# Kernel tuning notes

Measured on AMD Instinct MI355X. Metric: run time of the kernel, lower is better.

The kernel has to match this reference:

```python
import jax, jax.numpy as jnp
import numpy as np

BITS = 4
GROUP_SIZE = 128
INF, OUTF, TOKENS = 4096, 11008, 256


def setup_inputs() -> dict:
    key = jax.random.key(0)
    k1, k2, k3, k4, k5 = jax.random.split(key, 5)
    n_groups = INF // GROUP_SIZE  # 32
    x = jax.random.normal(k1, (TOKENS, INF), dtype=jnp.float32)
    qweight = jax.random.randint(k2, (INF // 32 * BITS, OUTF), 0, 2**31 - 1, dtype=jnp.int32)
    qzeros = jax.random.randint(k3, (n_groups, OUTF // 32 * BITS), 0, 2**31 - 1, dtype=jnp.int32)
    scales = jax.random.uniform(k4, (n_groups, OUTF), dtype=jnp.float32, minval=1e-3, maxval=2e-2)
    bias = jax.random.normal(k5, (OUTF,), dtype=jnp.float32)
    return {"x": x, "qweight": qweight, "qzeros": qzeros, "scales": scales, "bias": bias}


def _dequantize(qweight, qzeros, scales):
    """Unpack int4 nibbles and build the fp32 weight [infeatures, outfeatures]."""
    shifts = jnp.arange(0, 32, BITS, dtype=jnp.int32)  # [8]
    mask = (1 << BITS) - 1
    out_f = qweight.shape[1]
    # qweight row packs 8 consecutive in-features -> [K, O] int in [0, 15]
    w = ((qweight[:, None, :] >> shifts[None, :, None]) & mask).reshape(-1, out_f)
    # qzeros col packs 8 consecutive out-features; stored as (zero - 1)
    n_groups = qzeros.shape[0]
    z = (((qzeros[:, :, None] >> shifts[None, None, :]) & mask) + 1).reshape(n_groups, out_f)
    g_idx = jnp.arange(w.shape[0], dtype=jnp.int32) // GROUP_SIZE  # [K]
    return (w - z[g_idx]).astype(jnp.float32) * scales[g_idx]


def reference(x, qweight, qzeros, scales, bias):
    W = _dequantize(qweight, qzeros, scales)  # [infeatures, outfeatures]
    return x @ W + bias  # [tokens, outfeatures]
```

## Files before the change

kernel.cpp:

```cpp
#include <hip/hip_runtime.h>
#include <stdint.h>

#define TOKENS  256
#define INF     4096
#define OUTF    11008
#define NGROUPS 32
#define KSPLIT  2
#define PHK     128
#define NPH     ((INF / KSPLIT) / PHK)
#define NTH     256

typedef __attribute__((ext_vector_type(2))) _Float16 f16x2;
typedef __attribute__((ext_vector_type(8))) _Float16 f16x8;
typedef __attribute__((ext_vector_type(2))) __fp16   pkh2;
typedef __attribute__((ext_vector_type(4))) float    f32x4;

union U32H2 { uint32_t u; f16x2 h; };
union H8    { f16x2 h2[4]; f16x8 h8; };
union PK    { pkh2 p; f16x2 h; };

__device__ __forceinline__ void gl2lds16(const void* g, void* l) {
    __builtin_amdgcn_global_load_lds(
        (const __attribute__((address_space(1))) uint32_t*)g,
        (__attribute__((address_space(3))) uint32_t*)l, 16, 0, 0);
}

__global__ __launch_bounds__(NTH)
void prep(const float* __restrict__ x, _Float16* __restrict__ x16,
          const float* __restrict__ bias, float* __restrict__ out) {
    const int b = blockIdx.x;
    if (b < 512) {
        const int t   = b * NTH + threadIdx.x;
        const int row = t >> 9;
        const int c   = t & 511;
        const float* p = x + (size_t)row * INF + c * 8;
        f32x4 v0 = *(const f32x4*)p;
        f32x4 v1 = *(const f32x4*)(p + 4);
        H8 o; PK k0, k1, k2, k3;
        k0.p = __builtin_amdgcn_cvt_pkrtz(v0[0], v1[0]);
        k1.p = __builtin_amdgcn_cvt_pkrtz(v0[1], v1[1]);
        k2.p = __builtin_amdgcn_cvt_pkrtz(v0[2], v1[2]);
        k3.p = __builtin_amdgcn_cvt_pkrtz(v0[3], v1[3]);
        o.h2[0] = k0.h; o.h2[1] = k1.h; o.h2[2] = k2.h; o.h2[3] = k3.h;
        *(f16x8*)(x16 + (size_t)row * INF + c * 8) = o.h8;
    } else {
        const int t = (b - 512) * NTH + threadIdx.x;
        const int c = t % (OUTF / 4);
        const int r = t / (OUTF / 4);
        const f32x4 bv = ((const f32x4*)bias)[c];
        ((f32x4*)out)[(size_t)r * (OUTF / 4) + c] = bv;
    }
}

__global__ __launch_bounds__(NTH, 2)
void qlin_main(const _Float16* __restrict__ x16,
               const uint32_t* __restrict__ qweight,
               const uint32_t* __restrict__ qzeros,
               const float* __restrict__ scales,
               float* __restrict__ out)
{
    __shared__ alignas(16) _Float16 As[2][128 * PHK];

    const int tid = threadIdx.x;

    const int d   = blockIdx.x;
    const int lin = (d & 7) * 43 + (d >> 3);
    const int bx   = lin >> 2;
    const int memb = lin & 3;
    const int by = memb >> 1;
    const int ks = memb & 1;

    const int lane = tid & 63;
    const int quad = lane >> 4;
    const int l16  = lane & 15;
    const int wv   = tid >> 6;

    const int rowoff = tid >> 4;
    const int chk    = tid & 15;
    const int row0   = by * 128;
    const uint32_t aoff = (uint32_t)((row0 + rowoff) * (INF * 2)
                                     + ks * (INF / KSPLIT) * 2
                                     + ((chk ^ rowoff) & 15) * 16);
    const char* x16b = (const char*)x16;
    _Float16* ldsW = &As[0][0];
    const int ldsSlotBase = wv * 512;

    const int col0 = bx * 128 + wv * 32 + l16;
    const int col1 = col0 + 16;
    const int bOff0 = quad * OUTF + col0;
    const int bOff1 = quad * OUTF + col1;
    const int zsh   = (col0 & 7) * 4;
    const int qrow0 = ks * (INF / KSPLIT / 8);
    const int g0    = ks * (NGROUPS / KSPLIT);

    f32x4 acc[8][2];
#pragma unroll
    for (int mi = 0; mi < 8; ++mi)
#pragma unroll
        for (int nf = 0; nf < 2; ++nf)
            acc[mi][nf] = f32x4{0.f, 0.f, 0.f, 0.f};

    uint32_t Breg[2][8];
    float    sS[2][2];
    uint32_t qZ[2][2];

#pragma unroll
    for (int r = 0; r < 8; ++r)
        gl2lds16(x16b + aoff + r * 131072, ldsW + r * 2048 + ldsSlotBase);
    __builtin_amdgcn_sched_barrier(0);
    {
        sS[0][0] = scales[g0 * OUTF + col0];
        sS[0][1] = scales[g0 * OUTF + col1];
        qZ[0][0] = qzeros[g0 * (OUTF / 8) + (col0 >> 3)];
        qZ[0][1] = qzeros[g0 * (OUTF / 8) + (col1 >> 3)];
        const uint32_t* qp = qweight + (size_t)qrow0 * OUTF;
#pragma unroll
        for (int s = 0; s < 4; ++s) {
            Breg[0][2 * s + 0] = qp[(size_t)(s * 4) * OUTF + bOff0];
            Breg[0][2 * s + 1] = qp[(size_t)(s * 4) * OUTF + bOff1];
        }
    }

#define PHASE_BODY(PAR, P, DO_PREFETCH)                                          \
    {                                                                            \
        __builtin_amdgcn_sched_barrier(0);                                       \
        asm volatile("s_waitcnt vmcnt(12)" ::: "memory");                        \
        __builtin_amdgcn_s_barrier();                                            \
        __builtin_amdgcn_sched_barrier(0);                                       \
        if (DO_PREFETCH) {                                                       \
            const int pn = (P) + 1;                                              \
            const uint32_t pb = (uint32_t)(pn * (PHK * 2));                      \
            _Float16* ldsN = ldsW + (1 - (PAR)) * 16384;                         \
            _Pragma("unroll")                                                    \
            for (int r = 0; r < 8; ++r)                                          \
                gl2lds16(x16b + aoff + r * 131072 + pb,                          \
                         ldsN + r * 2048 + ldsSlotBase);                         \
            __builtin_amdgcn_sched_barrier(0);           \
            const int gn = g0 + pn;                                              \
            sS[1 - (PAR)][0] = scales[gn * OUTF + col0];                         \
            sS[1 - (PAR)][1] = scales[gn * OUTF + col1];                         \
            qZ[1 - (PAR)][0] = qzeros[gn * (OUTF / 8) + (col0 >> 3)];            \
            qZ[1 - (PAR)][1] = qzeros[gn * (OUTF / 8) + (col1 >> 3)];            \
            const uint32_t* qpb = qweight + (size_t)(qrow0 + pn * 16) * OUTF;    \
            _Pragma("unroll")                                                    \
            for (int s = 0; s < 4; ++s) {                                        \
                Breg[1 - (PAR)][2 * s + 0] = qpb[(size_t)(s * 4) * OUTF + bOff0];\
                Breg[1 - (PAR)][2 * s + 1] = qpb[(size_t)(s * 4) * OUTF + bOff1];\
            }                                                                    \
        }                                                                        \
        f16x2 hs2[2], hz2[2];                                                    \
        _Pragma("unroll")                                                        \
        for (int nf = 0; nf < 2; ++nf) {                                         \
            const float s = sS[PAR][nf];                                         \
            const int   z = (int)((qZ[PAR][nf] >> zsh) & 15u) + 1025;            \
            const _Float16 hs = (_Float16)s;                                     \
            const _Float16 hz = (_Float16)(-(float)z);                           \
            hs2[nf] = f16x2{hs, hs};                                             \
            hz2[nf] = f16x2{hz, hz};                                             \
        }                                                                        \
        const _Float16* buf = ldsW + (PAR) * 16384;                              \
        _Pragma("unroll")                                                        \
        for (int s = 0; s < 4; ++s) {                                            \
            f16x8 af[8];                                                         \
            _Pragma("unroll")                                                    \
            for (int mi = 0; mi < 8; ++mi) {                                     \
                const int m  = mi * 16 + l16;                                    \
                const int sc = ((s * 4 + quad) ^ l16) & 15;                      \
                af[mi] = *(const f16x8*)(buf + m * PHK + sc * 8);                \
            }                                                                    \
            _Pragma("unroll")                                                    \
            for (int nf = 0; nf < 2; ++nf) {                                     \
                const uint32_t q = Breg[PAR][2 * s + nf];                        \
                H8 b;                                                            \
                _Pragma("unroll")                                                \
                for (int j = 0; j < 4; ++j) {                                    \
                    U32H2 u;                                                     \
                    u.u = ((q >> (4 * j)) & 0x000F000Fu) | 0x64006400u;          \
                    b.h2[j] = (u.h + hz2[nf]) * hs2[nf];                         \
                }                                                                \
                __builtin_amdgcn_s_setprio(1);                                   \
                _Pragma("unroll")                                                \
                for (int mi = 0; mi < 8; ++mi)                                   \
                    acc[mi][nf] = __builtin_amdgcn_mfma_f32_16x16x32_f16(        \
                        af[mi], b.h8, acc[mi][nf], 0, 0, 0);                     \
                __builtin_amdgcn_s_setprio(0);                                   \
            }                                                                    \
        }                                                                        \
    }

#pragma unroll 1
    for (int pp = 0; pp < NPH / 2; ++pp) {
        PHASE_BODY(0, 2 * pp, true)
        PHASE_BODY(1, 2 * pp + 1, (pp < NPH / 2 - 1))
    }
#undef PHASE_BODY

#pragma unroll
    for (int nf = 0; nf < 2; ++nf) {
        const int col = (nf == 0) ? col0 : col1;
#pragma unroll
        for (int mi = 0; mi < 8; ++mi) {
            const int r0 = by * 128 + mi * 16 + quad * 4;
#pragma unroll
            for (int rg = 0; rg < 4; ++rg)
                unsafeAtomicAdd(&out[(size_t)(r0 + rg) * OUTF + col],
                                acc[mi][nf][rg]);
        }
    }
}

__global__ __launch_bounds__(NTH, 2)
void qlin_fb(const float* __restrict__ x,
             const uint32_t* __restrict__ qweight,
             const uint32_t* __restrict__ qzeros,
             const float* __restrict__ scales,
             const float* __restrict__ bias,
             float* __restrict__ out)
{
    __shared__ alignas(16) _Float16 Asb[64][40];
    __shared__ alignas(16) _Float16 Bsb[128][40];
    const int tid = threadIdx.x;
    const int bx = blockIdx.x, by = blockIdx.y;
    const int am = tid >> 2, ar = tid & 3;
    const float* xrow = x + (size_t)(by * 64 + am) * INF + ar * 8;
    const int bc = tid & 127, br = tid >> 7;
    const int bn = bx * 128 + bc;
    const int bswz = (bc >> 3) & 3;
    const int lane = tid & 63, quad = lane >> 4, l16 = lane & 15;
    const int wv = tid >> 6, wm = wv >> 1, wn = wv & 1;
    f32x4 acc[2][4];
#pragma unroll
    for (int i = 0; i < 2; ++i)
#pragma unroll
        for (int j = 0; j < 4; ++j) acc[i][j] = f32x4{0.f, 0.f, 0.f, 0.f};
    f32x4 pa0 = *(const f32x4*)(xrow + 0);
    f32x4 pa1 = *(const f32x4*)(xrow + 4);
    uint32_t pq0 = qweight[(size_t)br * OUTF + bn];
    uint32_t pq1 = qweight[(size_t)(br + 2) * OUTF + bn];
    for (int g = 0; g < NGROUPS; ++g) {
        const float s = scales[g * OUTF + bn];
        const uint32_t qzv = qzeros[g * (OUTF / 8) + (bn >> 3)];
        const int z = (int)((qzv >> (4 * (bn & 7))) & 15u) + 1;
        const _Float16 hs = (_Float16)s;
        const _Float16 hz = (_Float16)(-(float)(1024 + z));
        const f16x2 hs2 = {hs, hs}, hz2 = {hz, hz};
#pragma unroll
        for (int t4 = 0; t4 < 4; ++t4) {
            const int it = (g << 2) + t4;
            { H8 ah; PK p0, p1, p2, p3;
              p0.p = __builtin_amdgcn_cvt_pkrtz(pa0[0], pa1[0]);
              p1.p = __builtin_amdgcn_cvt_pkrtz(pa0[1], pa1[1]);
              p2.p = __builtin_amdgcn_cvt_pkrtz(pa0[2], pa1[2]);
              p3.p = __builtin_amdgcn_cvt_pkrtz(pa0[3], pa1[3]);
              ah.h2[0] = p0.h; ah.h2[1] = p1.h; ah.h2[2] = p2.h; ah.h2[3] = p3.h;
              *(f16x8*)&Asb[am][ar * 8] = ah.h8; }
            { const uint32_t qq[2] = {pq0, pq1};
#pragma unroll
              for (int rr = 0; rr < 2; ++rr) {
                  const int r = br + rr * 2; H8 bh;
#pragma unroll
                  for (int jp = 0; jp < 4; ++jp) {
                      U32H2 u; u.u = ((qq[rr] >> (4 * jp)) & 0x000F000Fu) | 0x64006400u;
                      bh.h2[jp] = (u.h + hz2) * hs2;
                  }
                  *(f16x8*)&Bsb[bc][(r ^ bswz) * 8] = bh.h8;
              } }
            __syncthreads();
            const int itn = (it < 127) ? it + 1 : 127;
            pa0 = *(const f32x4*)(xrow + itn * 32);
            pa1 = *(const f32x4*)(xrow + itn * 32 + 4);
            pq0 = qweight[(size_t)(itn * 4 + br) * OUTF + bn];
            pq1 = qweight[(size_t)(itn * 4 + br + 2) * OUTF + bn];
            f16x8 af[2], bf[4];
#pragma unroll
            for (int mi = 0; mi < 2; ++mi)
                af[mi] = *(const f16x8*)&Asb[wm * 32 + mi * 16 + l16][quad * 8];
#pragma unroll
            for (int ni = 0; ni < 4; ++ni) {
                const int c = wn * 64 + ni * 16 + l16;
                bf[ni] = *(const f16x8*)&Bsb[c][(quad ^ ((c >> 3) & 3)) * 8];
            }
#pragma unroll
            for (int mi = 0; mi < 2; ++mi)
#pragma unroll
                for (int ni = 0; ni < 4; ++ni)
                    acc[mi][ni] = __builtin_amdgcn_mfma_f32_16x16x32_f16(
                        af[mi], bf[ni], acc[mi][ni], 0, 0, 0);
            __syncthreads();
        }
    }
#pragma unroll
    for (int ni = 0; ni < 4; ++ni) {
        const int col = bx * 128 + wn * 64 + ni * 16 + l16;
        const float bv = bias[col];
#pragma unroll
        for (int mi = 0; mi < 2; ++mi) {
            const int row0 = by * 64 + wm * 32 + mi * 16 + quad * 4;
#pragma unroll
            for (int rg = 0; rg < 4; ++rg)
                out[(size_t)(row0 + rg) * OUTF + col] = acc[mi][ni][rg] + bv;
        }
    }
}

extern "C" void kernel_launch(void* const* d_in, const int* in_sizes, int n_in,
                              void* d_out, int out_size, void* d_ws, size_t ws_size,
                              hipStream_t stream) {
    const float*    xx = (const float*)d_in[0];
    const uint32_t* qw = (const uint32_t*)d_in[1];
    const uint32_t* qz = (const uint32_t*)d_in[2];
    const float*    sc = (const float*)d_in[3];
    const float*    bs = (const float*)d_in[4];
    float* out = (float*)d_out;

    const size_t x16_bytes = (size_t)TOKENS * INF * sizeof(_Float16);
    if (ws_size >= x16_bytes) {
        _Float16* x16 = (_Float16*)d_ws;
        prep<<<512 + (TOKENS * OUTF / 4) / NTH, NTH, 0, stream>>>(xx, x16, bs, out);
        qlin_main<<<(OUTF / 128) * (TOKENS / 128) * KSPLIT, NTH, 0, stream>>>(
            x16, qw, qz, sc, out);
    } else {
        dim3 grid(OUTF / 128, TOKENS / 64);
        qlin_fb<<<grid, NTH, 0, stream>>>(xx, qw, qz, sc, bs, out);
    }
}
```

Baseline: 123.1 us.

## Drop split-K; tile 64 columns per block with per-wave private A tiles

Removes the K-split and its atomic-add epilogue. Each block now covers 128 rows by 64 columns over the full K, and each wave owns 32 rows by 64 columns with its own LDS slice, so the block-wide barrier goes away. The bias is added in the epilogue, so the prep kernel no longer initialises the output. In exchange, each wave loads twice as many packed weights per phase, there is less A reuse per B dequant, and the launch uses the same block count with longer per-block work.

```diff
diff --git a/kernel.cpp b/kernel.cpp
--- a/kernel.cpp
+++ b/kernel.cpp
@@ -5,9 +5,8 @@
 #define INF     4096
 #define OUTF    11008
 #define NGROUPS 32
-#define KSPLIT  2
 #define PHK     128
-#define NPH     ((INF / KSPLIT) / PHK)
+#define NPH     32
 #define NTH     256
 
 typedef __attribute__((ext_vector_type(2))) _Float16 f16x2;
@@ -26,30 +25,20 @@
 }
 
 __global__ __launch_bounds__(NTH)
-void prep(const float* __restrict__ x, _Float16* __restrict__ x16,
-          const float* __restrict__ bias, float* __restrict__ out) {
-    const int b = blockIdx.x;
-    if (b < 512) {
-        const int t   = b * NTH + threadIdx.x;
-        const int row = t >> 9;
-        const int c   = t & 511;
-        const float* p = x + (size_t)row * INF + c * 8;
-        f32x4 v0 = *(const f32x4*)p;
-        f32x4 v1 = *(const f32x4*)(p + 4);
-        H8 o; PK k0, k1, k2, k3;
-        k0.p = __builtin_amdgcn_cvt_pkrtz(v0[0], v1[0]);
-        k1.p = __builtin_amdgcn_cvt_pkrtz(v0[1], v1[1]);
-        k2.p = __builtin_amdgcn_cvt_pkrtz(v0[2], v1[2]);
-        k3.p = __builtin_amdgcn_cvt_pkrtz(v0[3], v1[3]);
-        o.h2[0] = k0.h; o.h2[1] = k1.h; o.h2[2] = k2.h; o.h2[3] = k3.h;
-        *(f16x8*)(x16 + (size_t)row * INF + c * 8) = o.h8;
-    } else {
-        const int t = (b - 512) * NTH + threadIdx.x;
-        const int c = t % (OUTF / 4);
-        const int r = t / (OUTF / 4);
-        const f32x4 bv = ((const f32x4*)bias)[c];
-        ((f32x4*)out)[(size_t)r * (OUTF / 4) + c] = bv;
-    }
+void prep(const float* __restrict__ x, _Float16* __restrict__ x16) {
+    const int t   = blockIdx.x * NTH + threadIdx.x;
+    const int row = t >> 9;
+    const int c   = t & 511;
+    const float* p = x + (size_t)row * INF + c * 8;
+    f32x4 v0 = *(const f32x4*)p;
+    f32x4 v1 = *(const f32x4*)(p + 4);
+    H8 o; PK k0, k1, k2, k3;
+    k0.p = __builtin_amdgcn_cvt_pkrtz(v0[0], v1[0]);
+    k1.p = __builtin_amdgcn_cvt_pkrtz(v0[1], v1[1]);
+    k2.p = __builtin_amdgcn_cvt_pkrtz(v0[2], v1[2]);
+    k3.p = __builtin_amdgcn_cvt_pkrtz(v0[3], v1[3]);
+    o.h2[0] = k0.h; o.h2[1] = k1.h; o.h2[2] = k2.h; o.h2[3] = k3.h;
+    *(f16x8*)(x16 + (size_t)row * INF + c * 8) = o.h8;
 }
 
 __global__ __launch_bounds__(NTH, 2)
@@ -57,100 +46,95 @@
                const uint32_t* __restrict__ qweight,
                const uint32_t* __restrict__ qzeros,
                const float* __restrict__ scales,
+               const float* __restrict__ bias,
                float* __restrict__ out)
 {
-    __shared__ alignas(16) _Float16 As[2][128 * PHK];
+    __shared__ alignas(16) _Float16 As[4][2][4096];
 
     const int tid = threadIdx.x;
 
     const int d   = blockIdx.x;
     const int lin = (d & 7) * 43 + (d >> 3);
-    const int bx   = lin >> 2;
-    const int memb = lin & 3;
-    const int by = memb >> 1;
-    const int ks = memb & 1;
+    const int bx  = lin >> 1;
+    const int by  = lin & 1;
 
     const int lane = tid & 63;
     const int quad = lane >> 4;
     const int l16  = lane & 15;
     const int wv   = tid >> 6;
 
-    const int rowoff = tid >> 4;
-    const int chk    = tid & 15;
-    const int row0   = by * 128;
-    const uint32_t aoff = (uint32_t)((row0 + rowoff) * (INF * 2)
-                                     + ks * (INF / KSPLIT) * 2
-                                     + ((chk ^ rowoff) & 15) * 16);
     const char* x16b = (const char*)x16;
-    _Float16* ldsW = &As[0][0];
-    const int ldsSlotBase = wv * 512;
-
-    const int col0 = bx * 128 + wv * 32 + l16;
-    const int col1 = col0 + 16;
-    const int bOff0 = quad * OUTF + col0;
-    const int bOff1 = quad * OUTF + col1;
-    const int zsh   = (col0 & 7) * 4;
-    const int qrow0 = ks * (INF / KSPLIT / 8);
-    const int g0    = ks * (NGROUPS / KSPLIT);
-
-    f32x4 acc[8][2];
-#pragma unroll
-    for (int mi = 0; mi < 8; ++mi)
-#pragma unroll
-        for (int nf = 0; nf < 2; ++nf)
+    const char* aBase = x16b + (size_t)(by * 128 + wv * 32 + quad) * (INF * 2);
+    uint32_t co[4];
+#pragma unroll
+    for (int rm = 0; rm < 4; ++rm)
+        co[rm] = (uint32_t)(((l16 ^ ((quad + rm * 4) & 15)) & 15) * 16);
+
+    int colN[4], bOffN[4], zOffN[4];
+#pragma unroll
+    for (int nf = 0; nf < 4; ++nf) {
+        colN[nf]  = bx * 64 + nf * 16 + l16;
+        bOffN[nf] = quad * OUTF + colN[nf];
+        zOffN[nf] = colN[nf] >> 3;
+    }
+    const int zsh = (l16 & 7) * 4;
+
+    f32x4 acc[2][4];
+#pragma unroll
+    for (int mi = 0; mi < 2; ++mi)
+#pragma unroll
+        for (int nf = 0; nf < 4; ++nf)
             acc[mi][nf] = f32x4{0.f, 0.f, 0.f, 0.f};
 
-    uint32_t Breg[2][8];
-    float    sS[2][2];
-    uint32_t qZ[2][2];
-
-#pragma unroll
-    for (int r = 0; r < 8; ++r)
-        gl2lds16(x16b + aoff + r * 131072, ldsW + r * 2048 + ldsSlotBase);
+    uint32_t Breg[2][16];
+    float    sS[2][4];
+    uint32_t qZ[2][4];
+
+#define LOAD_A(PN, BUF)                                                          \
+    {                                                                            \
+        const uint32_t pb_ = (uint32_t)((PN) * (PHK * 2));                       \
+        _Pragma("unroll")                                                        \
+        for (int r = 0; r < 8; ++r)                                              \
+            gl2lds16(aBase + r * 32768 + pb_ + co[r & 3],                        \
+                     &As[wv][BUF][r * 512]);                                     \
+    }
+
+#define LOAD_B(SLOT, PN)                                                         \
+    {                                                                            \
+        const int gn_ = (PN);                                                    \
+        _Pragma("unroll")                                                        \
+        for (int nf = 0; nf < 4; ++nf) {                                         \
+            sS[SLOT][nf] = scales[gn_ * OUTF + colN[nf]];                        \
+            qZ[SLOT][nf] = qzeros[gn_ * (OUTF / 8) + zOffN[nf]];                 \
+        }                                                                        \
+        const uint32_t* qpb_ = qweight + (size_t)((PN) * 16) * OUTF;             \
+        _Pragma("unroll")                                                        \
+        for (int s_ = 0; s_ < 4; ++s_)                                           \
+            _Pragma("unroll")                                                    \
+            for (int nf = 0; nf < 4; ++nf)                                       \
+                Breg[SLOT][s_ * 4 + nf] =                                        \
+                    qpb_[(size_t)(s_ * 4) * OUTF + bOffN[nf]];                   \
+    }
+
+    LOAD_A(0, 0)
     __builtin_amdgcn_sched_barrier(0);
-    {
-        sS[0][0] = scales[g0 * OUTF + col0];
-        sS[0][1] = scales[g0 * OUTF + col1];
-        qZ[0][0] = qzeros[g0 * (OUTF / 8) + (col0 >> 3)];
-        qZ[0][1] = qzeros[g0 * (OUTF / 8) + (col1 >> 3)];
-        const uint32_t* qp = qweight + (size_t)qrow0 * OUTF;
-#pragma unroll
-        for (int s = 0; s < 4; ++s) {
-            Breg[0][2 * s + 0] = qp[(size_t)(s * 4) * OUTF + bOff0];
-            Breg[0][2 * s + 1] = qp[(size_t)(s * 4) * OUTF + bOff1];
-        }
-    }
-
-#define PHASE_BODY(PAR, P, DO_PREFETCH)                                          \
+    LOAD_B(0, 0)
+
+#define PHASE_BODY(PAR, P, DO_PRE, WAIT0)                                        \
     {                                                                            \
+        const int p_ = (P);                                                      \
         __builtin_amdgcn_sched_barrier(0);                                       \
-        asm volatile("s_waitcnt vmcnt(12)" ::: "memory");                        \
-        __builtin_amdgcn_s_barrier();                                            \
+        if (WAIT0) { asm volatile("s_waitcnt vmcnt(0)" ::: "memory"); }          \
+        else       { asm volatile("s_waitcnt vmcnt(24)" ::: "memory"); }         \
         __builtin_amdgcn_sched_barrier(0);                                       \
-        if (DO_PREFETCH) {                                                       \
-            const int pn = (P) + 1;                                              \
-            const uint32_t pb = (uint32_t)(pn * (PHK * 2));                      \
-            _Float16* ldsN = ldsW + (1 - (PAR)) * 16384;                         \
-            _Pragma("unroll")                                                    \
-            for (int r = 0; r < 8; ++r)                                          \
-                gl2lds16(x16b + aoff + r * 131072 + pb,                          \
-                         ldsN + r * 2048 + ldsSlotBase);                         \
+        if (DO_PRE) {                                                            \
+            LOAD_A(p_ + 1, 1 - (PAR))                                            \
             __builtin_amdgcn_sched_barrier(0);           \
-            const int gn = g0 + pn;                                              \
-            sS[1 - (PAR)][0] = scales[gn * OUTF + col0];                         \
-            sS[1 - (PAR)][1] = scales[gn * OUTF + col1];                         \
-            qZ[1 - (PAR)][0] = qzeros[gn * (OUTF / 8) + (col0 >> 3)];            \
-            qZ[1 - (PAR)][1] = qzeros[gn * (OUTF / 8) + (col1 >> 3)];            \
-            const uint32_t* qpb = qweight + (size_t)(qrow0 + pn * 16) * OUTF;    \
-            _Pragma("unroll")                                                    \
-            for (int s = 0; s < 4; ++s) {                                        \
-                Breg[1 - (PAR)][2 * s + 0] = qpb[(size_t)(s * 4) * OUTF + bOff0];\
-                Breg[1 - (PAR)][2 * s + 1] = qpb[(size_t)(s * 4) * OUTF + bOff1];\
-            }                                                                    \
+            LOAD_B(1 - (PAR), p_ + 1)                                            \
         }                                                                        \
-        f16x2 hs2[2], hz2[2];                                                    \
-        _Pragma("unroll")                                                        \
-        for (int nf = 0; nf < 2; ++nf) {                                         \
+        f16x2 hs2[4], hz2[4];                                                    \
+        _Pragma("unroll")                                                        \
+        for (int nf = 0; nf < 4; ++nf) {                                         \
             const float s = sS[PAR][nf];                                         \
             const int   z = (int)((qZ[PAR][nf] >> zsh) & 15u) + 1025;            \
             const _Float16 hs = (_Float16)s;                                     \
@@ -158,19 +142,19 @@
             hs2[nf] = f16x2{hs, hs};                                             \
             hz2[nf] = f16x2{hz, hz};                                             \
         }                                                                        \
-        const _Float16* buf = ldsW + (PAR) * 16384;                              \
+        const _Float16* buf = &As[wv][PAR][0];                                   \
         _Pragma("unroll")                                                        \
         for (int s = 0; s < 4; ++s) {                                            \
-            f16x8 af[8];                                                         \
+            f16x8 af[2];                                                         \
             _Pragma("unroll")                                                    \
-            for (int mi = 0; mi < 8; ++mi) {                                     \
-                const int m  = mi * 16 + l16;                                    \
+            for (int mi = 0; mi < 2; ++mi) {                                     \
+                const int w  = mi * 16 + l16;                                    \
                 const int sc = ((s * 4 + quad) ^ l16) & 15;                      \
-                af[mi] = *(const f16x8*)(buf + m * PHK + sc * 8);                \
+                af[mi] = *(const f16x8*)(buf + w * PHK + sc * 8);                \
             }                                                                    \
             _Pragma("unroll")                                                    \
-            for (int nf = 0; nf < 2; ++nf) {                                     \
-                const uint32_t q = Breg[PAR][2 * s + nf];                        \
+            for (int nf = 0; nf < 4; ++nf) {                                     \
+                const uint32_t q = Breg[PAR][s * 4 + nf];                        \
                 H8 b;                                                            \
                 _Pragma("unroll")                                                \
                 for (int j = 0; j < 4; ++j) {                                    \
@@ -180,7 +164,7 @@
                 }                                                                \
                 __builtin_amdgcn_s_setprio(1);                                   \
                 _Pragma("unroll")                                                \
-                for (int mi = 0; mi < 8; ++mi)                                   \
+                for (int mi = 0; mi < 2; ++mi)                                   \
                     acc[mi][nf] = __builtin_amdgcn_mfma_f32_16x16x32_f16(        \
                         af[mi], b.h8, acc[mi][nf], 0, 0, 0);                     \
                 __builtin_amdgcn_s_setprio(0);                                   \
@@ -189,22 +173,26 @@
     }
 
 #pragma unroll 1
-    for (int pp = 0; pp < NPH / 2; ++pp) {
-        PHASE_BODY(0, 2 * pp, true)
-        PHASE_BODY(1, 2 * pp + 1, (pp < NPH / 2 - 1))
-    }
+    for (int pp = 0; pp < NPH / 2 - 1; ++pp) {
+        PHASE_BODY(0, 2 * pp, true, false)
+        PHASE_BODY(1, 2 * pp + 1, true, false)
+    }
+    PHASE_BODY(0, NPH - 2, true,  false)
+    PHASE_BODY(1, NPH - 1, false, true)
 #undef PHASE_BODY
-
-#pragma unroll
-    for (int nf = 0; nf < 2; ++nf) {
-        const int col = (nf == 0) ? col0 : col1;
-#pragma unroll
-        for (int mi = 0; mi < 8; ++mi) {
-            const int r0 = by * 128 + mi * 16 + quad * 4;
+#undef LOAD_A
+#undef LOAD_B
+
+#pragma unroll
+    for (int nf = 0; nf < 4; ++nf) {
+        const int col = colN[nf];
+        const float bv = bias[col];
+#pragma unroll
+        for (int mi = 0; mi < 2; ++mi) {
+            const int r0 = by * 128 + wv * 32 + mi * 16 + quad * 4;
 #pragma unroll
             for (int rg = 0; rg < 4; ++rg)
-                unsafeAtomicAdd(&out[(size_t)(r0 + rg) * OUTF + col],
-                                acc[mi][nf][rg]);
+                out[(size_t)(r0 + rg) * OUTF + col] = acc[mi][nf][rg] + bv;
         }
     }
 }
@@ -316,9 +304,9 @@
     const size_t x16_bytes = (size_t)TOKENS * INF * sizeof(_Float16);
     if (ws_size >= x16_bytes) {
         _Float16* x16 = (_Float16*)d_ws;
-        prep<<<512 + (TOKENS * OUTF / 4) / NTH, NTH, 0, stream>>>(xx, x16, bs, out);
-        qlin_main<<<(OUTF / 128) * (TOKENS / 128) * KSPLIT, NTH, 0, stream>>>(
-            x16, qw, qz, sc, out);
+        prep<<<(TOKENS * INF / 8) / NTH, NTH, 0, stream>>>(xx, x16);
+        qlin_main<<<(OUTF / 64) * (TOKENS / 128), NTH, 0, stream>>>(
+            x16, qw, qz, sc, bs, out);
     } else {
         dim3 grid(OUTF / 128, TOKENS / 64);
         qlin_fb<<<grid, NTH, 0, stream>>>(xx, qw, qz, sc, bs, out);
```

Result: slower. 142.9 us (+16.0%).
